# Performance work log

Hardware: AMD Instinct MI355X
Metric: run time of the kernel (lower is better)

Reference implementation:

```python
import jax, jax.numpy as jnp
import numpy as np

B, L = 1, 2048
D_MODEL, D_STATE, D_CONV, EXPAND = 512, 16, 4, 2
D_INNER = D_MODEL * EXPAND
EPS = 1e-10  # clamp used by the torch reference


def setup_inputs() -> dict:
    key = jax.random.key(0)
    ks = jax.random.split(key, 8)
    s = lambda fan: 1.0 / np.sqrt(fan)
    x = jax.random.normal(ks[0], (B, L, D_MODEL), jnp.float32)
    # Weights stored in (in, out) layout: y = x @ W  (equivalent to torch Linear with W.T)
    W_in = jax.random.normal(ks[1], (D_MODEL, 2 * D_INNER), jnp.float32) * s(D_MODEL)
    conv_w = jax.random.normal(ks[2], (D_INNER, 1, D_CONV), jnp.float32) * s(D_CONV)  # depthwise (O, I/groups, K)
    conv_b = jax.random.normal(ks[3], (D_INNER,), jnp.float32) * 0.01
    W_xproj = jax.random.normal(ks[4], (D_INNER, 2 * D_STATE + 1), jnp.float32) * s(D_INNER)
    dt_w = jax.random.normal(ks[5], (D_INNER,), jnp.float32) * 0.1  # Linear(1, d_inner) weight, squeezed
    dt_b = jax.random.normal(ks[6], (D_INNER,), jnp.float32) * 0.1 - 2.0  # keep delta smallish
    A_log = jnp.log(jnp.arange(1, D_STATE + 1, dtype=jnp.float32))
    D = jnp.ones((D_INNER,), jnp.float32)
    W_out = jax.random.normal(ks[7], (D_INNER, D_MODEL), jnp.float32) * s(D_INNER)
    return {"x": x, "W_in": W_in, "conv_w": conv_w, "conv_b": conv_b,
            "W_xproj": W_xproj, "dt_w": dt_w, "dt_b": dt_b,
            "A_log": A_log, "D": D, "W_out": W_out}


def reference(x, W_in, conv_w, conv_b, W_xproj, dt_w, dt_b, A_log, D, W_out):
    d_inner, _, d_conv = conv_w.shape
    d_state = A_log.shape[0]

    xz = x @ W_in                                    # (B, L, 2*d_inner)
    xs, z = jnp.split(xz, 2, axis=-1)

    # Depthwise causal conv1d: left-pad d_conv-1 == torch pad-both + truncate to L
    xc = jnp.transpose(xs, (0, 2, 1))                # (B, d_inner, L)
    xc = jax.lax.conv_general_dilated(
        xc, conv_w, window_strides=(1,), padding=[(d_conv - 1, 0)],
        feature_group_count=d_inner,
        dimension_numbers=("NCH", "OIH", "NCH")) + conv_b[None, :, None]
    xs = jax.nn.silu(jnp.transpose(xc, (0, 2, 1)))   # (B, L, d_inner)

    xp = xs @ W_xproj                                # (B, L, 2*d_state+1)
    delta = jax.nn.softplus(xp[..., 0:1] * dt_w + dt_b)  # (B, L, d_inner)
    Bp = xp[..., 1:1 + d_state]                      # (B, L, d_state)
    Cp = xp[..., 1 + d_state:]                       # (B, L, d_state)
    A = -jnp.exp(A_log)                              # (d_state,)

    # --- parallel selective scan via cumulative log-sum (faithful to source) ---
    A_bar = jnp.exp(delta[..., None] * A)                            # (B,L,Di,S)
    BX = delta[..., None] * Bp[:, :, None, :] * xs[..., None]        # (B,L,Di,S)
    log_A_bar = jnp.log(jnp.maximum(A_bar, EPS))
    A_cumsum = jnp.exp(jnp.cumsum(log_A_bar, axis=1))
    A_shift = jnp.concatenate([jnp.ones_like(A_cumsum[:, :1]), A_cumsum[:, :-1]], axis=1)
    weighted_BX = BX / jnp.maximum(A_shift, EPS)
    h = A_cumsum * jnp.cumsum(weighted_BX, axis=1) / jnp.maximum(A_bar, EPS)
    y = jnp.einsum("bls,blds->bld", Cp, h) + D * xs                  # (B,L,Di)

    y = y * jax.nn.silu(z)
    return y @ W_out                                                  # (B,L,D)
```

## Files before the change

kernel.cpp:

```cpp
#include <hip/hip_runtime.h>
#include <hip/hip_bf16.h>


#define L_SEQ 2048
#define DM 512
#define DI 1024
#define DS 16
#define NXP 33
#define EPS 1e-10f
#define RCPEPS 1e10f
#define LOG2E 1.44269504088896340736f
#define LN2 0.69314718055994530942f
#define LOG2EPS -33.219280948873623478f

typedef __hip_bfloat16 bf16;
typedef __attribute__((ext_vector_type(8))) short bf16x8v;
typedef __attribute__((ext_vector_type(4))) float f32x4v;
typedef __attribute__((ext_vector_type(4))) unsigned int u32x4v;

__device__ __forceinline__ void st1(float* p, float v) { *p = v; }
__device__ __forceinline__ void st1(bf16* p, float v) { *p = __float2bfloat16(v); }

__device__ __forceinline__ float fexp2(float x) { return __builtin_amdgcn_exp2f(x); }
__device__ __forceinline__ float frcp(float x) { return __builtin_amdgcn_rcpf(x); }

__device__ __forceinline__ void load8(const float* p, float* v) {
  float4 a = *(const float4*)p;
  float4 b = *(const float4*)(p + 4);
  v[0] = a.x; v[1] = a.y; v[2] = a.z; v[3] = a.w;
  v[4] = b.x; v[5] = b.y; v[6] = b.z; v[7] = b.w;
}

__global__ __launch_bounds__(256)
void transpose_cast_kernel(const float* __restrict__ W, bf16* __restrict__ WT,
                           int R, int C) {
  __shared__ float tile[32][33];
  int c0 = blockIdx.x * 32, r0 = blockIdx.y * 32;
  int tx = threadIdx.x & 31, ty = threadIdx.x >> 5;
#pragma unroll
  for (int i = 0; i < 4; ++i) {
    int rr = ty + i * 8;
    tile[rr][tx] = W[(size_t)(r0 + rr) * C + c0 + tx];
  }
  __syncthreads();
#pragma unroll
  for (int i = 0; i < 4; ++i) {
    int cc = ty + i * 8;
    WT[(size_t)(c0 + cc) * R + r0 + tx] = __float2bfloat16(tile[tx][cc]);
  }
}

__global__ __launch_bounds__(256)
void cast_f32_bf16_kernel(const float* __restrict__ src, bf16* __restrict__ dst,
                          int n8) {
  int i = blockIdx.x * 256 + threadIdx.x;
  if (i < n8) {
    float v[8];
    load8(src + (size_t)i * 8, v);
    bf16 o[8];
#pragma unroll
    for (int j = 0; j < 8; ++j) o[j] = __float2bfloat16(v[j]);
    *(uint4*)(dst + (size_t)i * 8) = *(uint4*)o;
  }
}

template <int WM, int WN, typename TC>
__global__ __launch_bounds__(256)
void gemm_gl(const bf16* __restrict__ A, const bf16* __restrict__ BT,
             TC* __restrict__ C, int K, int lda, int ldc) {
  constexpr int BM = 2 * WM * 16, BN = 2 * WN * 16;
  __shared__ __align__(16) bf16 As[2][BM * 32];
  __shared__ __align__(16) bf16 Bs[2][BN * 32];
  const int tid = threadIdx.x;
  const int wave = tid >> 6, lane = tid & 63;
  const int q = lane >> 4, r = lane & 15;
  const int wr = wave >> 1, wc = wave & 1;
  const int row0 = blockIdx.y * BM, col0 = blockIdx.x * BN;
  f32x4v acc[WM][WN] = {};
  const int nt = K / 32;

  auto stage = [&](int buf, int t) {
    int k0 = t * 32;
#pragma unroll
    for (int i = 0; i < BM / 64; ++i) {
      int slot = tid + i * 256;
      int row = slot >> 2, seg = slot & 3;
      __builtin_amdgcn_global_load_lds(
          (const __attribute__((address_space(1))) void*)(
              A + (size_t)(row0 + row) * lda + k0 + seg * 8),
          (__attribute__((address_space(3))) void*)&As[buf][row * 32 + seg * 8],
          16, 0, 0);
    }
#pragma unroll
    for (int i = 0; i < BN / 64; ++i) {
      int slot = tid + i * 256;
      int row = slot >> 2, seg = slot & 3;
      __builtin_amdgcn_global_load_lds(
          (const __attribute__((address_space(1))) void*)(
              BT + (size_t)(col0 + row) * K + k0 + seg * 8),
          (__attribute__((address_space(3))) void*)&Bs[buf][row * 32 + seg * 8],
          16, 0, 0);
    }
  };

  stage(0, 0);
  __syncthreads();
  int cur = 0;
  for (int t = 0; t < nt; ++t) {
    if (t + 1 < nt) stage(cur ^ 1, t + 1);
    bf16x8v a[WM], b[WN];
#pragma unroll
    for (int m = 0; m < WM; ++m)
      a[m] = *(const bf16x8v*)&As[cur][(wr * WM * 16 + m * 16 + r) * 32 + q * 8];
#pragma unroll
    for (int n = 0; n < WN; ++n)
      b[n] = *(const bf16x8v*)&Bs[cur][(wc * WN * 16 + n * 16 + r) * 32 + q * 8];
#pragma unroll
    for (int m = 0; m < WM; ++m)
#pragma unroll
      for (int n = 0; n < WN; ++n)
        acc[m][n] = __builtin_amdgcn_mfma_f32_16x16x32_bf16(a[m], b[n],
                                                            acc[m][n], 0, 0, 0);
    __syncthreads();
    cur ^= 1;
  }
#pragma unroll
  for (int m = 0; m < WM; ++m)
#pragma unroll
    for (int n = 0; n < WN; ++n)
#pragma unroll
      for (int reg = 0; reg < 4; ++reg) {
        int mm = row0 + wr * WM * 16 + m * 16 + q * 4 + reg;
        int nn = col0 + wc * WN * 16 + n * 16 + r;
        st1(C + (size_t)mm * ldc + nn, acc[m][n][reg]);
      }
}

__global__ __launch_bounds__(256)
void gemm_xproj(const bf16* __restrict__ A, const float* __restrict__ Wx,
                float* __restrict__ xpcT) {
  __shared__ __align__(16) bf16 As[64 * 40];
  __shared__ __align__(16) bf16 Bs[64 * 40];
  const int tid = threadIdx.x;
  const int wave = tid >> 6, lane = tid & 63;
  const int q = lane >> 4, r = lane & 15;
  const int row0 = blockIdx.y * 64;
  const int srow = tid >> 2, sseg = tid & 3;
  f32x4v acc[4] = {};
  for (int k0 = 0; k0 < DI; k0 += 32) {
    *(uint4*)&As[srow * 40 + sseg * 8] =
        *(const uint4*)(A + (size_t)(row0 + srow) * DI + k0 + sseg * 8);
    int k = tid >> 3, n0 = (tid & 7) * 8;
#pragma unroll
    for (int j = 0; j < 8; ++j) {
      int n = n0 + j;
      float v = (n < NXP) ? Wx[(size_t)(k0 + k) * NXP + n] : 0.f;
      Bs[n * 40 + k] = __float2bfloat16(v);
    }
    __syncthreads();
    bf16x8v a = *(const bf16x8v*)&As[(wave * 16 + r) * 40 + q * 8];
#pragma unroll
    for (int j = 0; j < 4; ++j) {
      bf16x8v b = *(const bf16x8v*)&Bs[(j * 16 + r) * 40 + q * 8];
      acc[j] = __builtin_amdgcn_mfma_f32_16x16x32_bf16(a, b, acc[j], 0, 0, 0);
    }
    __syncthreads();
  }
#pragma unroll
  for (int j = 0; j < 4; ++j)
#pragma unroll
    for (int reg = 0; reg < 4; ++reg) {
      int m = row0 + wave * 16 + q * 4 + reg;
      int n = j * 16 + r;
      if (n < NXP) xpcT[(size_t)n * L_SEQ + m] = acc[j][reg];
    }
}

__global__ __launch_bounds__(256)
void conv_silu_dual(const bf16* __restrict__ xz, const float* __restrict__ conv_w,
                    const float* __restrict__ conv_b, bf16* __restrict__ xs,
                    bf16* __restrict__ xsT) {
  __shared__ bf16 tile[67][72];
  __shared__ bf16 sout[64][72];
  const int tid = threadIdx.x;
  const int d0 = blockIdx.x * 64, l0 = blockIdx.y * 64;
  for (int slot = tid; slot < 67 * 8; slot += 256) {
    int rr = slot >> 3, seg = slot & 7;
    int l = l0 - 3 + rr;
    uint4 v = {0, 0, 0, 0};
    if (l >= 0) v = *(const uint4*)(xz + (size_t)l * (2 * DI) + d0 + seg * 8);
    *(uint4*)&tile[rr][seg * 8] = v;
  }
  __syncthreads();
  {
    int lr = tid >> 3, c0t = (tid & 7) * 8;
#pragma unroll
    for (int half = 0; half < 2; ++half) {
      int lrow = lr + half * 32;
      bf16 o[8];
#pragma unroll
      for (int j = 0; j < 8; ++j) {
        int c = c0t + j;
        float acc = conv_b[d0 + c];
#pragma unroll
        for (int k = 0; k < 4; ++k)
          acc = fmaf(__bfloat162float(tile[lrow + k][c]), conv_w[(d0 + c) * 4 + k], acc);
        float v = acc / (1.f + __expf(-acc));
        o[j] = __float2bfloat16(v);
        sout[c][lrow] = o[j];
      }
      *(uint4*)(xs + (size_t)(l0 + lrow) * DI + d0 + c0t) = *(uint4*)o;
    }
  }
  __syncthreads();
  for (int slot = tid; slot < 64 * 8; slot += 256) {
    int dd = slot >> 3, seg = slot & 7;
    *(uint4*)(xsT + (size_t)(d0 + dd) * L_SEQ + l0 + seg * 8) =
        *(uint4*)&sout[dd][seg * 8];
  }
}

__global__ __launch_bounds__(256)
void gate_transpose_kernel(const bf16* __restrict__ yT, const bf16* __restrict__ zbuf,
                           int ldz, bf16* __restrict__ ys) {
  __shared__ bf16 tile[64][72];
  int d0 = blockIdx.y * 64, l0 = blockIdx.x * 64;
#pragma unroll
  for (int it = 0; it < 2; ++it) {
    int slot = threadIdx.x + it * 256;
    int dd = slot >> 3, seg = slot & 7;
    *(uint4*)&tile[dd][seg * 8] = *(const uint4*)(yT + (size_t)(d0 + dd) * L_SEQ + l0 + seg * 8);
  }
  __syncthreads();
#pragma unroll
  for (int it = 0; it < 2; ++it) {
    int slot = threadIdx.x + it * 256;
    int ll = slot >> 3, seg = slot & 7;
    bf16 zt[8];
    *(uint4*)zt = *(const uint4*)(zbuf + (size_t)(l0 + ll) * ldz + d0 + seg * 8);
    bf16 o[8];
#pragma unroll
    for (int j = 0; j < 8; ++j) {
      float yv = __bfloat162float(tile[seg * 8 + j][ll]);
      float zv = __bfloat162float(zt[j]);
      o[j] = __float2bfloat16(yv * zv * frcp(1.f + fexp2(-zv * LOG2E)));
    }
    *(uint4*)(ys + (size_t)(l0 + ll) * DI + d0 + seg * 8) = *(uint4*)o;
  }
}

#define LC 512
#define NW 16
#define SPW 32
#define PSX 513
#define LCP 516

__global__ __launch_bounds__(1024)
void scan_kernel(bf16* __restrict__ xsT, const float* __restrict__ xpcT,
                 const float* __restrict__ dt_w, const float* __restrict__ dt_b,
                 const float* __restrict__ A_log, const float* __restrict__ Dvec) {
  __shared__ float sxpT[NXP * PSX];
  __shared__ float sdt[4 * LCP], sg[4 * LCP], sxs[4 * LCP];
  __shared__ float sys[4 * LCP];
  __shared__ float Wtot[NW][64], Vtot[NW][64];
  const int tid = threadIdx.x;
  const int wave = tid >> 6, lane = tid & 63;
  const int s = lane & 15, dl = lane >> 4;
  const int d0 = blockIdx.x * 4;
  const int base = wave * SPW;
  const float As2 = -expf(A_log[s]) * LOG2E;
  const float Dd = Dvec[d0 + dl];
  float dtw[4], dtb[4];
#pragma unroll
  for (int c = 0; c < 4; ++c) {
    dtw[c] = dt_w[d0 + c];
    dtb[c] = dt_b[d0 + c];
  }
  float cs2_carry = 0.f, S_carry = 0.f;
  for (int l0 = 0; l0 < L_SEQ; l0 += LC) {
    for (int idx = tid; idx < NXP * LC; idx += 1024) {
      int u = __builtin_amdgcn_readfirstlane(idx & ~63);
      int j = u >> 9, lb = u & (LC - 1);
      const float* gp = xpcT + (size_t)j * L_SEQ + l0 + lb + lane;
      __builtin_amdgcn_global_load_lds(
          (const __attribute__((address_space(1))) void*)gp,
          (__attribute__((address_space(3))) void*)&sxpT[j * PSX + lb], 4, 0, 0);
    }
    for (int slot = tid; slot < 4 * (LC / 8); slot += 1024) {
      int c = slot >> 6, seg = slot & 63;
      bf16 tmp[8];
      *(uint4*)tmp = *(const uint4*)(xsT + (size_t)(d0 + c) * L_SEQ + l0 + seg * 8);
#pragma unroll
      for (int j = 0; j < 8; ++j) sxs[c * LCP + seg * 8 + j] = __bfloat162float(tmp[j]);
    }
    __syncthreads();
    for (int idx = tid; idx < 4 * LC; idx += 1024) {
      int c = idx >> 9, i = idx & (LC - 1);
      float x0 = sxpT[i];
      float a = fmaf(x0, dtw[c], dtb[c]);
      float dt = __log2f(1.f + fexp2(a * LOG2E)) * LN2;
      sdt[c * LCP + i] = dt;
      sg[c * LCP + i] = dt * sxs[c * LCP + i];
    }
    __syncthreads();
    float P[SPW];
    float Wl = 0.f;
#pragma unroll
    for (int k = 0; k < SPW; ++k) {
      float u = sdt[dl * LCP + base + k] * As2;
      P[k] = Wl;
      Wl += fmaxf(u, LOG2EPS);
    }
    Wtot[wave][lane] = Wl;
    __syncthreads();
    float O = cs2_carry, Wall = 0.f;
    for (int w = 0; w < NW; ++w) {
      float t = Wtot[w][lane];
      if (w < wave) O += t;
      Wall += t;
    }
    float Vl = 0.f;
#pragma unroll
    for (int k = 0; k < SPW; ++k) {
      float rcpA = fminf(fexp2(-(O + P[k])), RCPEPS);
      float gb = sg[dl * LCP + base + k] * sxpT[(1 + s) * PSX + base + k];
      Vl = fmaf(gb, rcpA, Vl);
    }
    Vtot[wave][lane] = Vl;
    __syncthreads();
    float SO = S_carry, Vall = 0.f;
    for (int w = 0; w < NW; ++w) {
      float tv = Vtot[w][lane];
      if (w < wave) SO += tv;
      Vall += tv;
    }
    float S = SO;
#pragma unroll
    for (int k = 0; k < SPW; ++k) {
      float xk = O + P[k];
      float rcpA = fminf(fexp2(-xk), RCPEPS);
      float aprev = fexp2(xk);
      float gb = sg[dl * LCP + base + k] * sxpT[(1 + s) * PSX + base + k];
      S = fmaf(gb, rcpA, S);
      float h = aprev * S;
      float contrib = sxpT[(17 + s) * PSX + base + k] * h;
      contrib += __shfl_xor(contrib, 8);
      contrib += __shfl_xor(contrib, 4);
      contrib += __shfl_xor(contrib, 2);
      contrib += __shfl_xor(contrib, 1);
      if (s == 0)
        sys[dl * LCP + base + k] = contrib + Dd * sxs[dl * LCP + base + k];
    }
    cs2_carry += Wall;
    S_carry += Vall;
    __syncthreads();
    for (int slot = tid; slot < 4 * (LC / 8); slot += 1024) {
      int c = slot >> 6, seg = slot & 63;
      bf16 tmp[8];
#pragma unroll
      for (int j = 0; j < 8; ++j) tmp[j] = __float2bfloat16(sys[c * LCP + seg * 8 + j]);
      u32x4v vv;
      vv.x = ((unsigned int*)tmp)[0]; vv.y = ((unsigned int*)tmp)[1];
      vv.z = ((unsigned int*)tmp)[2]; vv.w = ((unsigned int*)tmp)[3];
      __builtin_nontemporal_store(vv,
          (u32x4v*)(xsT + (size_t)(d0 + c) * L_SEQ + l0 + seg * 8));
    }
  }
}

extern "C" void kernel_launch(void* const* d_in, const int* in_sizes, int n_in,
                              void* d_out, int out_size, void* d_ws, size_t ws_size,
                              hipStream_t stream) {
  const float* x       = (const float*)d_in[0];
  const float* W_in    = (const float*)d_in[1];
  const float* conv_w  = (const float*)d_in[2];
  const float* conv_b  = (const float*)d_in[3];
  const float* W_xproj = (const float*)d_in[4];
  const float* dt_w    = (const float*)d_in[5];
  const float* dt_b    = (const float*)d_in[6];
  const float* A_log   = (const float*)d_in[7];
  const float* Dvec    = (const float*)d_in[8];
  const float* W_out   = (const float*)d_in[9];
  float* out = (float*)d_out;

  char* ws = (char*)d_ws;
  const size_t MB = 1024 * 1024;
  bf16* xz    = (bf16*)(ws);
  bf16* buf1  = (bf16*)(ws + 8 * MB);
  bf16* WinT  = (bf16*)(ws + 12 * MB);
  bf16* xbf   = (bf16*)(ws + 14 * MB);
  bf16* xsT   = (bf16*)(ws + 12 * MB);
  bf16* WoutT = (bf16*)(ws + 12 * MB);
  float* xpcT = (float*)(ws + 16 * MB);

  transpose_cast_kernel<<<dim3(2 * DI / 32, DM / 32), 256, 0, stream>>>(
      W_in, WinT, DM, 2 * DI);
  cast_f32_bf16_kernel<<<dim3(L_SEQ * DM / (256 * 8)), 256, 0, stream>>>(
      x, xbf, L_SEQ * DM / 8);
  gemm_gl<4, 4, bf16><<<dim3(2 * DI / 128, L_SEQ / 128), 256, 0, stream>>>(
      xbf, WinT, xz, DM, DM, 2 * DI);
  conv_silu_dual<<<dim3(DI / 64, L_SEQ / 64), 256, 0, stream>>>(
      xz, conv_w, conv_b, buf1, xsT);
  gemm_xproj<<<dim3(1, L_SEQ / 64), 256, 0, stream>>>(buf1, W_xproj, xpcT);
  scan_kernel<<<DI / 4, 1024, 0, stream>>>(xsT, xpcT, dt_w, dt_b, A_log, Dvec);
  gate_transpose_kernel<<<dim3(L_SEQ / 64, DI / 64), 256, 0, stream>>>(
      xsT, xz + DI, 2 * DI, buf1);
  transpose_cast_kernel<<<dim3(DM / 32, DI / 32), 256, 0, stream>>>(
      W_out, WoutT, DI, DM);
  gemm_gl<2, 2, float><<<dim3(DM / 64, L_SEQ / 64), 256, 0, stream>>>(
      buf1, WoutT, out, DI, DI, DM);
}
```

Measured before the change: 218.6 us.

## Split-K xproj GEMM with atomics and merge prep/transpose kernels into fewer launches

The xproj GEMM is split over K into 8 blocks per row tile and combined with float atomicAdd, with the output zeroed inside the conv kernel. This raises parallelism from only 32 blocks. The W_in transpose and x cast are merged into one launch, and the W_out transpose is folded into the gating kernel, removing two launches. Atomics make the summation order nondeterministic and add atomic traffic.

```diff
diff --git a/kernel.cpp b/kernel.cpp
--- a/kernel.cpp
+++ b/kernel.cpp
@@ -32,35 +32,32 @@
 }
 
 __global__ __launch_bounds__(256)
-void transpose_cast_kernel(const float* __restrict__ W, bf16* __restrict__ WT,
-                           int R, int C) {
+void prep_kernel(const float* __restrict__ W_in, bf16* __restrict__ WinT,
+                 const float* __restrict__ x, bf16* __restrict__ xbf) {
   __shared__ float tile[32][33];
-  int c0 = blockIdx.x * 32, r0 = blockIdx.y * 32;
-  int tx = threadIdx.x & 31, ty = threadIdx.x >> 5;
-#pragma unroll
-  for (int i = 0; i < 4; ++i) {
-    int rr = ty + i * 8;
-    tile[rr][tx] = W[(size_t)(r0 + rr) * C + c0 + tx];
-  }
-  __syncthreads();
-#pragma unroll
-  for (int i = 0; i < 4; ++i) {
-    int cc = ty + i * 8;
-    WT[(size_t)(c0 + cc) * R + r0 + tx] = __float2bfloat16(tile[tx][cc]);
-  }
-}
-
-__global__ __launch_bounds__(256)
-void cast_f32_bf16_kernel(const float* __restrict__ src, bf16* __restrict__ dst,
-                          int n8) {
-  int i = blockIdx.x * 256 + threadIdx.x;
-  if (i < n8) {
+  int b = blockIdx.x;
+  if (b < 1024) {
+    int c0 = (b & 63) * 32, r0 = (b >> 6) * 32;
+    int tx = threadIdx.x & 31, ty = threadIdx.x >> 5;
+#pragma unroll
+    for (int i = 0; i < 4; ++i) {
+      int rr = ty + i * 8;
+      tile[rr][tx] = W_in[(size_t)(r0 + rr) * (2 * DI) + c0 + tx];
+    }
+    __syncthreads();
+#pragma unroll
+    for (int i = 0; i < 4; ++i) {
+      int cc = ty + i * 8;
+      WinT[(size_t)(c0 + cc) * DM + r0 + tx] = __float2bfloat16(tile[tx][cc]);
+    }
+  } else {
+    int i = (b - 1024) * 256 + threadIdx.x;
     float v[8];
-    load8(src + (size_t)i * 8, v);
+    load8(x + (size_t)i * 8, v);
     bf16 o[8];
 #pragma unroll
     for (int j = 0; j < 8; ++j) o[j] = __float2bfloat16(v[j]);
-    *(uint4*)(dst + (size_t)i * 8) = *(uint4*)o;
+    *(uint4*)(xbf + (size_t)i * 8) = *(uint4*)o;
   }
 }
 
@@ -137,17 +134,18 @@
 }
 
 __global__ __launch_bounds__(256)
-void gemm_xproj(const bf16* __restrict__ A, const float* __restrict__ Wx,
-                float* __restrict__ xpcT) {
+void gemm_xproj_sk(const bf16* __restrict__ A, const float* __restrict__ Wx,
+                   float* __restrict__ xpcT) {
   __shared__ __align__(16) bf16 As[64 * 40];
   __shared__ __align__(16) bf16 Bs[64 * 40];
   const int tid = threadIdx.x;
   const int wave = tid >> 6, lane = tid & 63;
   const int q = lane >> 4, r = lane & 15;
   const int row0 = blockIdx.y * 64;
+  const int kb = blockIdx.x * 128;
   const int srow = tid >> 2, sseg = tid & 3;
   f32x4v acc[4] = {};
-  for (int k0 = 0; k0 < DI; k0 += 32) {
+  for (int k0 = kb; k0 < kb + 128; k0 += 32) {
     *(uint4*)&As[srow * 40 + sseg * 8] =
         *(const uint4*)(A + (size_t)(row0 + srow) * DI + k0 + sseg * 8);
     int k = tid >> 3, n0 = (tid & 7) * 8;
@@ -172,18 +170,22 @@
     for (int reg = 0; reg < 4; ++reg) {
       int m = row0 + wave * 16 + q * 4 + reg;
       int n = j * 16 + r;
-      if (n < NXP) xpcT[(size_t)n * L_SEQ + m] = acc[j][reg];
+      if (n < NXP) atomicAdd(&xpcT[(size_t)n * L_SEQ + m], acc[j][reg]);
     }
 }
 
 __global__ __launch_bounds__(256)
 void conv_silu_dual(const bf16* __restrict__ xz, const float* __restrict__ conv_w,
                     const float* __restrict__ conv_b, bf16* __restrict__ xs,
-                    bf16* __restrict__ xsT) {
+                    bf16* __restrict__ xsT, float* __restrict__ xpcT) {
   __shared__ bf16 tile[67][72];
   __shared__ bf16 sout[64][72];
   const int tid = threadIdx.x;
   const int d0 = blockIdx.x * 64, l0 = blockIdx.y * 64;
+  {
+    int zb = blockIdx.y * gridDim.x + blockIdx.x;
+    if (tid < 132) xpcT[(size_t)zb * 132 + tid] = 0.f;
+  }
   for (int slot = tid; slot < 67 * 8; slot += 256) {
     int rr = slot >> 3, seg = slot & 7;
     int l = l0 - 3 + rr;
@@ -221,9 +223,28 @@
 }
 
 __global__ __launch_bounds__(256)
-void gate_transpose_kernel(const bf16* __restrict__ yT, const bf16* __restrict__ zbuf,
-                           int ldz, bf16* __restrict__ ys) {
+void gate_wt_kernel(const bf16* __restrict__ yT, const bf16* __restrict__ zbuf,
+                    int ldz, bf16* __restrict__ ys,
+                    const float* __restrict__ W_out, bf16* __restrict__ WoutT) {
   __shared__ bf16 tile[64][72];
+  __shared__ float ttile[32][33];
+  if (blockIdx.y >= 16) {
+    int tb = (blockIdx.y - 16) * 32 + blockIdx.x;
+    int c0 = (tb & 15) * 32, r0 = (tb >> 4) * 32;
+    int tx = threadIdx.x & 31, ty = threadIdx.x >> 5;
+#pragma unroll
+    for (int i = 0; i < 4; ++i) {
+      int rr = ty + i * 8;
+      ttile[rr][tx] = W_out[(size_t)(r0 + rr) * DM + c0 + tx];
+    }
+    __syncthreads();
+#pragma unroll
+    for (int i = 0; i < 4; ++i) {
+      int cc = ty + i * 8;
+      WoutT[(size_t)(c0 + cc) * DI + r0 + tx] = __float2bfloat16(ttile[tx][cc]);
+    }
+    return;
+  }
   int d0 = blockIdx.y * 64, l0 = blockIdx.x * 64;
 #pragma unroll
   for (int it = 0; it < 2; ++it) {
@@ -390,23 +411,18 @@
   bf16* WinT  = (bf16*)(ws + 12 * MB);
   bf16* xbf   = (bf16*)(ws + 14 * MB);
   bf16* xsT   = (bf16*)(ws + 12 * MB);
-  bf16* WoutT = (bf16*)(ws + 12 * MB);
   float* xpcT = (float*)(ws + 16 * MB);
-
-  transpose_cast_kernel<<<dim3(2 * DI / 32, DM / 32), 256, 0, stream>>>(
-      W_in, WinT, DM, 2 * DI);
-  cast_f32_bf16_kernel<<<dim3(L_SEQ * DM / (256 * 8)), 256, 0, stream>>>(
-      x, xbf, L_SEQ * DM / 8);
+  bf16* WoutT = (bf16*)(ws + 16 * MB);
+
+  prep_kernel<<<dim3(1536), 256, 0, stream>>>(W_in, WinT, x, xbf);
   gemm_gl<4, 4, bf16><<<dim3(2 * DI / 128, L_SEQ / 128), 256, 0, stream>>>(
       xbf, WinT, xz, DM, DM, 2 * DI);
   conv_silu_dual<<<dim3(DI / 64, L_SEQ / 64), 256, 0, stream>>>(
-      xz, conv_w, conv_b, buf1, xsT);
-  gemm_xproj<<<dim3(1, L_SEQ / 64), 256, 0, stream>>>(buf1, W_xproj, xpcT);
+      xz, conv_w, conv_b, buf1, xsT, xpcT);
+  gemm_xproj_sk<<<dim3(8, L_SEQ / 64), 256, 0, stream>>>(buf1, W_xproj, xpcT);
   scan_kernel<<<DI / 4, 1024, 0, stream>>>(xsT, xpcT, dt_w, dt_b, A_log, Dvec);
-  gate_transpose_kernel<<<dim3(L_SEQ / 64, DI / 64), 256, 0, stream>>>(
-      xsT, xz + DI, 2 * DI, buf1);
-  transpose_cast_kernel<<<dim3(DM / 32, DI / 32), 256, 0, stream>>>(
-      W_out, WoutT, DI, DM);
+  gate_wt_kernel<<<dim3(L_SEQ / 64, 2 * DI / 64), 256, 0, stream>>>(
+      xsT, xz + DI, 2 * DI, buf1, W_out, WoutT);
   gemm_gl<2, 2, float><<<dim3(DM / 64, L_SEQ / 64), 256, 0, stream>>>(
       buf1, WoutT, out, DI, DI, DM);
 }
```

After: 191.5 us, median of 3. 12.4% less time.
